# Kernel optimization log

Hardware: AMD Instinct MI355X
Metric: run time of the kernel (lower is better)

The kernel has to match this reference:

```python
import jax, jax.numpy as jnp
import numpy as np

N, E, D, L = 50000, 625000, 128, 7
EPS = 1e-7   # GENConv message epsilon
T = 1.0      # softmax aggregation temperature (learn_t=False)
NUM_ATOM_FEATS, ATOM_VOCAB = 9, 64
NUM_BOND_FEATS, BOND_VOCAB = 3, 8


def setup_inputs() -> dict:
    key = jax.random.key(0)
    ks = jax.random.split(key, 9)
    x = jax.random.randint(ks[0], (N, NUM_ATOM_FEATS), 0, ATOM_VOCAB, dtype=jnp.int32)
    edge_index = jax.random.randint(ks[1], (2, E), 0, N, dtype=jnp.int32)
    edge_attr = jax.random.randint(ks[2], (E, NUM_BOND_FEATS), 0, BOND_VOCAB, dtype=jnp.int32)
    atom_emb = jax.random.normal(ks[3], (NUM_ATOM_FEATS, ATOM_VOCAB, D), dtype=jnp.float32) * 0.1
    bond_emb = jax.random.normal(ks[4], (NUM_BOND_FEATS, BOND_VOCAB, D), dtype=jnp.float32) * 0.1
    W = jax.random.normal(ks[5], (L, D, D), dtype=jnp.float32) / np.sqrt(D).astype(np.float32)
    b = jnp.zeros((L, D), dtype=jnp.float32)
    ln_gamma = jnp.ones((L, D), dtype=jnp.float32)
    ln_beta = jnp.zeros((L, D), dtype=jnp.float32)
    return dict(x=x, edge_index=edge_index, edge_attr=edge_attr,
                atom_emb=atom_emb, bond_emb=bond_emb, W=W, b=b,
                ln_gamma=ln_gamma, ln_beta=ln_beta)


def _layer_norm(h, g, bta):
    mu = jnp.mean(h, axis=-1, keepdims=True)
    var = jnp.var(h, axis=-1, keepdims=True)
    return (h - mu) * jax.lax.rsqrt(var + 1e-5) * g + bta


def _gen_conv(h, src, dst, edge_emb, Wl, bl):
    # GENConv: msg = relu(x_j + e) + eps; softmax aggregation over dst; Linear(x + m)
    msg = jax.nn.relu(h[src] + edge_emb) + EPS                 # [E, D]
    logits = msg * T
    seg_max = jax.ops.segment_max(logits, dst, num_segments=N)  # [N, D]
    seg_max = jnp.where(jnp.isfinite(seg_max), seg_max, 0.0)    # empty segments
    e = jnp.exp(logits - seg_max[dst])                          # [E, D]
    denom = jax.ops.segment_sum(e, dst, num_segments=N)         # [N, D]
    alpha = e / (denom[dst] + 1e-16)
    m = jax.ops.segment_sum(alpha * msg, dst, num_segments=N)   # [N, D]
    return (h + m) @ Wl + bl


def reference(x, edge_index, edge_attr, atom_emb, bond_emb, W, b, ln_gamma, ln_beta):
    src, dst = edge_index[0], edge_index[1]
    # AtomEncoder: sum of per-feature embedding lookups -> [N, D]
    h = jnp.sum(atom_emb[jnp.arange(NUM_ATOM_FEATS)[None, :], x], axis=1)
    # BondEncoder (conv_encode_edge=False: encoded once) -> [E, D]
    edge_emb = jnp.sum(bond_emb[jnp.arange(NUM_BOND_FEATS)[None, :], edge_attr], axis=1)
    # res+ block, dropout=0 (no-op)
    h = _gen_conv(h, src, dst, edge_emb, W[0], b[0])
    for layer in range(1, L):
        h2 = jax.nn.relu(_layer_norm(h, ln_gamma[layer - 1], ln_beta[layer - 1]))
        h = _gen_conv(h2, src, dst, edge_emb, W[layer], b[layer]) + h
    h = _layer_norm(h, ln_gamma[L - 1], ln_beta[L - 1])
    return h
```

## Files before the change

kernel.cpp:

```cpp
#include <hip/hip_runtime.h>
#include <hip/hip_fp16.h>
#include <math.h>


constexpr int D = 128;
constexpr int NA = 9;
constexpr int NB = 3;


__global__ void k_hist(const int* __restrict__ dst, int* __restrict__ deg, int E) {
    int e = blockIdx.x * 256 + threadIdx.x;
    if (e < E) atomicAdd(&deg[dst[e]], 1);
}

__global__ void k_scan_a(const int* __restrict__ deg, int* __restrict__ offs,
                         int* __restrict__ bsum, int N) {
    __shared__ int s[256];
    int i = blockIdx.x * 256 + threadIdx.x;
    int v = (i < N) ? deg[i] : 0;
    s[threadIdx.x] = v;
    __syncthreads();
    for (int d = 1; d < 256; d <<= 1) {
        int add = (threadIdx.x >= d) ? s[threadIdx.x - d] : 0;
        __syncthreads();
        s[threadIdx.x] += add;
        __syncthreads();
    }
    if (i < N) offs[i + 1] = s[threadIdx.x];
    if (threadIdx.x == 255) bsum[blockIdx.x] = s[255];
    if (i == 0) offs[0] = 0;
}

__global__ void k_scan_b(const int* __restrict__ bsum, int* __restrict__ bexc, int nb) {
    __shared__ int s[256];
    int t = threadIdx.x;
    int v = (t < nb) ? bsum[t] : 0;
    s[t] = v;
    __syncthreads();
    for (int d = 1; d < 256; d <<= 1) {
        int add = (t >= d) ? s[t - d] : 0;
        __syncthreads();
        s[t] += add;
        __syncthreads();
    }
    if (t < nb) bexc[t] = s[t] - v;
}

__global__ void k_scan_c(int* __restrict__ offs, const int* __restrict__ bexc, int N) {
    int i = blockIdx.x * 256 + threadIdx.x;
    if (i < N) offs[i + 1] += bexc[blockIdx.x];
}

__global__ void k_fill(const int* __restrict__ src, const int* __restrict__ dst,
                       const int* __restrict__ attr, const int* __restrict__ offs,
                       int* __restrict__ cur, int2* __restrict__ recs, int E) {
    int e = blockIdx.x * 256 + threadIdx.x;
    if (e >= E) return;
    int d = dst[e];
    int pos = offs[d] + atomicAdd(&cur[d], 1);
    int cidx = attr[e * 3] * 64 + attr[e * 3 + 1] * 8 + attr[e * 3 + 2];
    recs[pos] = make_int2(src[e], cidx);
}

__global__ void k_comb(const float* __restrict__ bemb, __half* __restrict__ comb16) {
    int gid = blockIdx.x * 256 + threadIdx.x;
    int c = gid >> 5, q = gid & 31;
    int a0 = c >> 6, a1 = (c >> 3) & 7, a2 = c & 7;
    float4 v0 = *(const float4*)(bemb + (a0)*D + q * 4);
    float4 v1 = *(const float4*)(bemb + (8 + a1) * D + q * 4);
    float4 v2 = *(const float4*)(bemb + (16 + a2) * D + q * 4);
    __half2* c2 = (__half2*)comb16;
    c2[c * 64 + q * 2]     = __floats2half2_rn(v0.x + v1.x + v2.x, v0.y + v1.y + v2.y);
    c2[c * 64 + q * 2 + 1] = __floats2half2_rn(v0.z + v1.z + v2.z, v0.w + v1.w + v2.w);
}


__global__ void k_atom(const int* __restrict__ x, const float* __restrict__ aemb,
                       __half* __restrict__ h16, int N) {
    int wid = (blockIdx.x * blockDim.x + threadIdx.x) >> 6;
    int lane = threadIdx.x & 63;
    if (wid >= N) return;
    const int* xr = x + wid * NA;
    float ax = 0.f, ay = 0.f;
#pragma unroll
    for (int f = 0; f < NA; ++f) {
        int v = xr[f];
        const float2 e = *(const float2*)(aemb + (f * 64 + v) * D + 2 * lane);
        ax += e.x; ay += e.y;
    }
    ((__half2*)h16)[wid * 64 + lane] = __floats2half2_rn(ax, ay);
}


__global__ __launch_bounds__(256) void k_agg(const __half* __restrict__ h16,
                      const int2* __restrict__ recs,
                      const int* __restrict__ offs, const __half* __restrict__ comb16,
                      __half* __restrict__ t16, int N) {
    int wid = (blockIdx.x * blockDim.x + threadIdx.x) >> 6;
    int lane = threadIdx.x & 63;
    if (wid >= N) return;
    int su = __builtin_amdgcn_readfirstlane(offs[wid]);
    int eu = __builtin_amdgcn_readfirstlane(offs[wid + 1]);
    __half2 hm2 = ((const __half2*)h16)[wid * 64 + lane];
    float2 hme = make_float2(__low2float(hm2), __high2float(hm2));
    if (su >= eu) {
        ((__half2*)t16)[wid * 64 + lane] = hm2;
        return;
    }
    constexpr float L2E = 1.4426950408889634f;
    float Sx = 0.f, Sy = 0.f, Wx = 0.f, Wy = 0.f;
    int last = eu - 1;

    const __half2* hrow = (const __half2*)h16 + lane;
    const __half2* crow = (const __half2*)comb16 + lane;

    __half2 ha[4], ca[4], hb[4], cb[4];

    auto loadg = [&](int gb, __half2* hs, __half2* cs) {
#pragma unroll
        for (int i = 0; i < 4; ++i) {
            int idx = gb + i; idx = (idx < last) ? idx : last;
            int2 rr = recs[idx];
            int sj = __builtin_amdgcn_readfirstlane(rr.x);
            int cj = __builtin_amdgcn_readfirstlane(rr.y);
            hs[i] = hrow[sj * 64];
            cs[i] = crow[cj * 64];
        }
    };
    auto compg = [&](int gb, const __half2* hs, const __half2* cs) {
        float px[4], py[4], vx[4], vy[4];
#pragma unroll
        for (int i = 0; i < 4; ++i) {
            float hx = __low2float(hs[i]), hy = __high2float(hs[i]);
            float cx = __low2float(cs[i]), cy = __high2float(cs[i]);
            vx[i] = fmaxf(hx + cx, 0.f) + 1e-7f;
            vy[i] = fmaxf(hy + cy, 0.f) + 1e-7f;
            bool valid = (gb + i) < eu;
            float uxv = valid ? vx[i] * L2E : -INFINITY;
            float uyv = valid ? vy[i] * L2E : -INFINITY;
            px[i] = __builtin_amdgcn_exp2f(uxv);
            py[i] = __builtin_amdgcn_exp2f(uyv);
        }
        Sx += (px[0] + px[1]) + (px[2] + px[3]);
        Sy += (py[0] + py[1]) + (py[2] + py[3]);
        Wx += fmaf(px[0], vx[0], px[1] * vx[1]) + fmaf(px[2], vx[2], px[3] * vx[3]);
        Wy += fmaf(py[0], vy[0], py[1] * vy[1]) + fmaf(py[2], vy[2], py[3] * vy[3]);
    };

    loadg(su, ha, ca);
    loadg(su + 4, hb, cb);
    for (int e = su; e < eu; e += 8) {
        compg(e, ha, ca);
        loadg(e + 8, ha, ca);
        compg(e + 4, hb, cb);
        loadg(e + 12, hb, cb);
    }
    float mx = Wx / (Sx + 1e-16f);
    float my = Wy / (Sy + 1e-16f);
    ((__half2*)t16)[wid * 64 + lane] = __floats2half2_rn(hme.x + mx, hme.y + my);
}


template <int MODE>
__global__ __launch_bounds__(256) void k_gemm(const __half* __restrict__ A16,
                                              const float* __restrict__ Wl,
                                              const float* __restrict__ bl,
                                              const __half* __restrict__ res16,
                                              __half* __restrict__ hres16,
                                              const float* __restrict__ g,
                                              const float* __restrict__ bta,
                                              __half* __restrict__ h16,
                                              float* __restrict__ out,
                                              int N, int useRes) {
    __shared__ float As[32 * 132];
    __shared__ float Bs[32 * 128];
    int tid = threadIdx.x;
    int tx = tid & 15;
    int ty = tid >> 4;
    int m0 = blockIdx.x * 128;

    float acc[8][8];
#pragma unroll
    for (int i = 0; i < 8; ++i)
#pragma unroll
        for (int j = 0; j < 8; ++j) acc[i][j] = 0.f;

    for (int kk0 = 0; kk0 < 128; kk0 += 32) {
#pragma unroll
        for (int it = 0; it < 2; ++it) {
            int lin = it * 256 + tid;
            int node = lin >> 2, kq = lin & 3;
            int gm = m0 + node;
            float4 raw = make_float4(0.f, 0.f, 0.f, 0.f);
            if (gm < N) raw = *(const float4*)(A16 + gm * 128 + kk0 + kq * 8);
            const __half2* hp = (const __half2*)&raw;
#pragma unroll
            for (int j = 0; j < 4; ++j) {
                float2 f = make_float2(__low2float(hp[j]), __high2float(hp[j]));
                As[(kq * 8 + 2 * j) * 132 + node]     = f.x;
                As[(kq * 8 + 2 * j + 1) * 132 + node] = f.y;
            }
        }
#pragma unroll
        for (int it = 0; it < 4; ++it) {
            int lin = it * 256 + tid;
            int k = lin >> 5, jq = lin & 31;
            *(float4*)(Bs + k * 128 + jq * 4) = *(const float4*)(Wl + (kk0 + k) * 128 + jq * 4);
        }
        __syncthreads();
#pragma unroll
        for (int kk = 0; kk < 32; ++kk) {
            float4 a_lo = *(const float4*)(As + kk * 132 + ty * 8);
            float4 a_hi = *(const float4*)(As + kk * 132 + ty * 8 + 4);
            float2 bv[4];
#pragma unroll
            for (int jj = 0; jj < 4; ++jj)
                bv[jj] = *(const float2*)(Bs + kk * 128 + tx * 2 + 32 * jj);
            float am[8] = {a_lo.x, a_lo.y, a_lo.z, a_lo.w,
                           a_hi.x, a_hi.y, a_hi.z, a_hi.w};
#pragma unroll
            for (int i = 0; i < 8; ++i)
#pragma unroll
                for (int jj = 0; jj < 4; ++jj) {
                    acc[i][2 * jj]     = fmaf(am[i], bv[jj].x, acc[i][2 * jj]);
                    acc[i][2 * jj + 1] = fmaf(am[i], bv[jj].y, acc[i][2 * jj + 1]);
                }
        }
        __syncthreads();
    }

    float2 bb[4], gg[4], bt[4];
#pragma unroll
    for (int jj = 0; jj < 4; ++jj) {
        bb[jj] = *(const float2*)(bl + tx * 2 + 32 * jj);
        gg[jj] = *(const float2*)(g + tx * 2 + 32 * jj);
        bt[jj] = *(const float2*)(bta + tx * 2 + 32 * jj);
    }
#pragma unroll
    for (int i = 0; i < 8; ++i) {
        int gm = m0 + ty * 8 + i;
        bool ok = gm < N;
        float o[8];
#pragma unroll
        for (int jj = 0; jj < 4; ++jj) {
            o[2 * jj]     = acc[i][2 * jj] + bb[jj].x;
            o[2 * jj + 1] = acc[i][2 * jj + 1] + bb[jj].y;
        }
        if (useRes && ok) {
#pragma unroll
            for (int jj = 0; jj < 4; ++jj) {
                __half2 rr = *(const __half2*)(res16 + gm * 128 + tx * 2 + 32 * jj);
                o[2 * jj]     += __low2float(rr);
                o[2 * jj + 1] += __high2float(rr);
            }
        }
        if (MODE == 0 && ok) {
#pragma unroll
            for (int jj = 0; jj < 4; ++jj)
                *(__half2*)(hres16 + gm * 128 + tx * 2 + 32 * jj) =
                    __floats2half2_rn(o[2 * jj], o[2 * jj + 1]);
        }
        float s = 0.f, ss = 0.f;
#pragma unroll
        for (int j = 0; j < 8; ++j) { s += o[j]; ss += o[j] * o[j]; }
#pragma unroll
        for (int off = 1; off < 16; off <<= 1) {
            s += __shfl_xor(s, off, 64);
            ss += __shfl_xor(ss, off, 64);
        }
        float mu = s * (1.f / 128.f);
        float var = ss * (1.f / 128.f) - mu * mu;
        float rs = rsqrtf(var + 1e-5f);
        float l[8];
#pragma unroll
        for (int jj = 0; jj < 4; ++jj) {
            l[2 * jj]     = (o[2 * jj] - mu) * rs * gg[jj].x + bt[jj].x;
            l[2 * jj + 1] = (o[2 * jj + 1] - mu) * rs * gg[jj].y + bt[jj].y;
        }
        if (MODE == 0) {
#pragma unroll
            for (int j = 0; j < 8; ++j) l[j] = fmaxf(l[j], 0.f);
            if (ok) {
                __half2* hrow = (__half2*)h16 + gm * 64;
#pragma unroll
                for (int jj = 0; jj < 4; ++jj)
                    hrow[tx + 16 * jj] = __floats2half2_rn(l[2 * jj], l[2 * jj + 1]);
            }
        } else {
            if (ok) {
#pragma unroll
                for (int jj = 0; jj < 4; ++jj)
                    *(float2*)(out + gm * 128 + tx * 2 + 32 * jj) =
                        make_float2(l[2 * jj], l[2 * jj + 1]);
            }
        }
    }
}


extern "C" void kernel_launch(void* const* d_in, const int* in_sizes, int n_in,
                              void* d_out, int out_size, void* d_ws, size_t ws_size,
                              hipStream_t stream) {
    const int*   x    = (const int*)d_in[0];
    const int*   ei   = (const int*)d_in[1];
    const int*   attr = (const int*)d_in[2];
    const float* aemb = (const float*)d_in[3];
    const float* bemb = (const float*)d_in[4];
    const float* Wf   = (const float*)d_in[5];
    const float* bf   = (const float*)d_in[6];
    const float* gam  = (const float*)d_in[7];
    const float* bet  = (const float*)d_in[8];
    float* out = (float*)d_out;

    const int N = in_sizes[0] / NA;
    const int E = in_sizes[1] / 2;
    const int L = in_sizes[5] / (D * D);

    char* ws = (char*)d_ws;
    size_t o = 0;
    auto carve = [&](size_t bytes) -> void* {
        void* p = (void*)(ws + o);
        o += (bytes + 255) & ~(size_t)255;
        return p;
    };
    __half* hres16 = (__half*)carve((size_t)N * D * 2);
    __half* h16    = (__half*)carve((size_t)N * D * 2);
    __half* t16    = (__half*)carve((size_t)N * D * 2);
    int2*   recs   = (int2*)carve((size_t)E * 8);
    __half* comb16 = (__half*)carve(512 * D * 2);
    int*    deg    = (int*)carve((size_t)N * 4);
    int*    cur    = (int*)carve((size_t)N * 4);
    int*    offs   = (int*)carve((size_t)(N + 1) * 4);
    int*    bsum   = (int*)carve(4096);
    int*    bexc   = (int*)carve(4096);

    const int* src = ei;
    const int* dst = ei + E;

    hipMemsetAsync(deg, 0, (size_t)N * 4, stream);
    hipMemsetAsync(cur, 0, (size_t)N * 4, stream);

    int ebl = (E + 255) / 256;
    int nbl = (N + 255) / 256;
    k_comb<<<64, 256, 0, stream>>>(bemb, comb16);
    k_hist<<<ebl, 256, 0, stream>>>(dst, deg, E);
    k_scan_a<<<nbl, 256, 0, stream>>>(deg, offs, bsum, N);
    k_scan_b<<<1, 256, 0, stream>>>(bsum, bexc, nbl);
    k_scan_c<<<nbl, 256, 0, stream>>>(offs, bexc, N);
    k_fill<<<ebl, 256, 0, stream>>>(src, dst, attr, offs, cur, recs, E);

    int wbl = (N * 64 + 255) / 256;
    k_atom<<<wbl, 256, 0, stream>>>(x, aemb, h16, N);

    int gbl = (N + 127) / 128;
    for (int l = 0; l < L; ++l) {
        k_agg<<<wbl, 256, 0, stream>>>(h16, recs, offs, comb16, t16, N);
        if (l == L - 1) {
            k_gemm<1><<<gbl, 256, 0, stream>>>(t16, Wf + l * D * D, bf + l * D,
                                               hres16, hres16,
                                               gam + l * D, bet + l * D, h16, out,
                                               N, 1);
        } else {
            k_gemm<0><<<gbl, 256, 0, stream>>>(t16, Wf + l * D * D, bf + l * D,
                                               hres16, hres16,
                                               gam + l * D, bet + l * D, h16, out,
                                               N, l > 0 ? 1 : 0);
        }
    }
}
```

Before: 673.3 us.

## Replace FP32 SIMT GEMM with FP16 MFMA GEMM using pre-transposed half weights

Rewrites the per-layer linear+LayerNorm kernel to use 16x16x32 FP16 MFMA instructions. Each wave handles 16 nodes and computes all 128 output features from register-resident A fragments, with weights read directly from a pre-transposed FP16 copy instead of staged through shared memory. A new setup kernel converts and transposes all layer weights to half once per launch. This removes the scalar FMA work and the LDS staging, at the cost of FP16 weight precision and uncached global weight reads per wave.

```diff
diff --git a/kernel.cpp b/kernel.cpp
--- a/kernel.cpp
+++ b/kernel.cpp
@@ -6,6 +6,9 @@
 constexpr int D = 128;
 constexpr int NA = 9;
 constexpr int NB = 3;
+
+using half8  = __attribute__((ext_vector_type(8))) _Float16;
+using floatx4 = __attribute__((ext_vector_type(4))) float;
 
 
 __global__ void k_hist(const int* __restrict__ dst, int* __restrict__ deg, int E) {
@@ -72,6 +75,15 @@
     __half2* c2 = (__half2*)comb16;
     c2[c * 64 + q * 2]     = __floats2half2_rn(v0.x + v1.x + v2.x, v0.y + v1.y + v2.y);
     c2[c * 64 + q * 2 + 1] = __floats2half2_rn(v0.z + v1.z + v2.z, v0.w + v1.w + v2.w);
+}
+
+__global__ void k_wt(const float* __restrict__ W, __half* __restrict__ Wt16, int total) {
+    int o = blockIdx.x * 256 + threadIdx.x;
+    if (o >= total) return;
+    int l = o >> 14;
+    int rem = o & 16383;
+    int f = rem >> 7, k = rem & 127;
+    Wt16[o] = __float2half_rn(W[(l << 14) + k * 128 + f]);
 }
 
 
@@ -163,7 +175,7 @@
 
 template <int MODE>
 __global__ __launch_bounds__(256) void k_gemm(const __half* __restrict__ A16,
-                                              const float* __restrict__ Wl,
+                                              const __half* __restrict__ Wt16,
                                               const float* __restrict__ bl,
                                               const __half* __restrict__ res16,
                                               __half* __restrict__ hres16,
@@ -172,127 +184,85 @@
                                               __half* __restrict__ h16,
                                               float* __restrict__ out,
                                               int N, int useRes) {
-    __shared__ float As[32 * 132];
-    __shared__ float Bs[32 * 128];
-    int tid = threadIdx.x;
-    int tx = tid & 15;
-    int ty = tid >> 4;
-    int m0 = blockIdx.x * 128;
-
-    float acc[8][8];
-#pragma unroll
-    for (int i = 0; i < 8; ++i)
-#pragma unroll
-        for (int j = 0; j < 8; ++j) acc[i][j] = 0.f;
-
-    for (int kk0 = 0; kk0 < 128; kk0 += 32) {
-#pragma unroll
-        for (int it = 0; it < 2; ++it) {
-            int lin = it * 256 + tid;
-            int node = lin >> 2, kq = lin & 3;
-            int gm = m0 + node;
-            float4 raw = make_float4(0.f, 0.f, 0.f, 0.f);
-            if (gm < N) raw = *(const float4*)(A16 + gm * 128 + kk0 + kq * 8);
-            const __half2* hp = (const __half2*)&raw;
-#pragma unroll
-            for (int j = 0; j < 4; ++j) {
-                float2 f = make_float2(__low2float(hp[j]), __high2float(hp[j]));
-                As[(kq * 8 + 2 * j) * 132 + node]     = f.x;
-                As[(kq * 8 + 2 * j + 1) * 132 + node] = f.y;
-            }
-        }
-#pragma unroll
-        for (int it = 0; it < 4; ++it) {
-            int lin = it * 256 + tid;
-            int k = lin >> 5, jq = lin & 31;
-            *(float4*)(Bs + k * 128 + jq * 4) = *(const float4*)(Wl + (kk0 + k) * 128 + jq * 4);
-        }
-        __syncthreads();
-#pragma unroll
-        for (int kk = 0; kk < 32; ++kk) {
-            float4 a_lo = *(const float4*)(As + kk * 132 + ty * 8);
-            float4 a_hi = *(const float4*)(As + kk * 132 + ty * 8 + 4);
-            float2 bv[4];
-#pragma unroll
-            for (int jj = 0; jj < 4; ++jj)
-                bv[jj] = *(const float2*)(Bs + kk * 128 + tx * 2 + 32 * jj);
-            float am[8] = {a_lo.x, a_lo.y, a_lo.z, a_lo.w,
-                           a_hi.x, a_hi.y, a_hi.z, a_hi.w};
-#pragma unroll
-            for (int i = 0; i < 8; ++i)
-#pragma unroll
-                for (int jj = 0; jj < 4; ++jj) {
-                    acc[i][2 * jj]     = fmaf(am[i], bv[jj].x, acc[i][2 * jj]);
-                    acc[i][2 * jj + 1] = fmaf(am[i], bv[jj].y, acc[i][2 * jj + 1]);
-                }
-        }
-        __syncthreads();
-    }
-
-    float2 bb[4], gg[4], bt[4];
-#pragma unroll
-    for (int jj = 0; jj < 4; ++jj) {
-        bb[jj] = *(const float2*)(bl + tx * 2 + 32 * jj);
-        gg[jj] = *(const float2*)(g + tx * 2 + 32 * jj);
-        bt[jj] = *(const float2*)(bta + tx * 2 + 32 * jj);
-    }
-#pragma unroll
-    for (int i = 0; i < 8; ++i) {
-        int gm = m0 + ty * 8 + i;
-        bool ok = gm < N;
-        float o[8];
-#pragma unroll
-        for (int jj = 0; jj < 4; ++jj) {
-            o[2 * jj]     = acc[i][2 * jj] + bb[jj].x;
-            o[2 * jj + 1] = acc[i][2 * jj + 1] + bb[jj].y;
-        }
-        if (useRes && ok) {
-#pragma unroll
-            for (int jj = 0; jj < 4; ++jj) {
-                __half2 rr = *(const __half2*)(res16 + gm * 128 + tx * 2 + 32 * jj);
-                o[2 * jj]     += __low2float(rr);
-                o[2 * jj + 1] += __high2float(rr);
-            }
-        }
-        if (MODE == 0 && ok) {
-#pragma unroll
-            for (int jj = 0; jj < 4; ++jj)
-                *(__half2*)(hres16 + gm * 128 + tx * 2 + 32 * jj) =
-                    __floats2half2_rn(o[2 * jj], o[2 * jj + 1]);
-        }
-        float s = 0.f, ss = 0.f;
-#pragma unroll
-        for (int j = 0; j < 8; ++j) { s += o[j]; ss += o[j] * o[j]; }
-#pragma unroll
-        for (int off = 1; off < 16; off <<= 1) {
-            s += __shfl_xor(s, off, 64);
-            ss += __shfl_xor(ss, off, 64);
-        }
-        float mu = s * (1.f / 128.f);
-        float var = ss * (1.f / 128.f) - mu * mu;
-        float rs = rsqrtf(var + 1e-5f);
-        float l[8];
-#pragma unroll
-        for (int jj = 0; jj < 4; ++jj) {
-            l[2 * jj]     = (o[2 * jj] - mu) * rs * gg[jj].x + bt[jj].x;
-            l[2 * jj + 1] = (o[2 * jj + 1] - mu) * rs * gg[jj].y + bt[jj].y;
-        }
+    int lane = threadIdx.x & 63;
+    int wave = threadIdx.x >> 6;
+    int quad = lane >> 4, col = lane & 15;
+    int node = blockIdx.x * 64 + wave * 16 + col;
+    bool nok = node < N;
+    int nc = nok ? node : N - 1;
+
+    const __half* arow = A16 + (size_t)nc * 128;
+    half8 bfrag[4];
+#pragma unroll
+    for (int ks = 0; ks < 4; ++ks)
+        bfrag[ks] = *(const half8*)(arow + ks * 32 + quad * 8);
+
+    floatx4 acc[8];
+#pragma unroll
+    for (int ft = 0; ft < 8; ++ft) acc[ft] = (floatx4){0.f, 0.f, 0.f, 0.f};
+
+#pragma unroll
+    for (int ft = 0; ft < 8; ++ft) {
+        const __half* wrow = Wt16 + (size_t)(ft * 16 + col) * 128;
+#pragma unroll
+        for (int ks = 0; ks < 4; ++ks) {
+            half8 afrag = *(const half8*)(wrow + ks * 32 + quad * 8);
+            acc[ft] = __builtin_amdgcn_mfma_f32_16x16x32_f16(afrag, bfrag[ks],
+                                                             acc[ft], 0, 0, 0);
+        }
+    }
+
+    float s = 0.f, ss = 0.f;
+#pragma unroll
+    for (int ft = 0; ft < 8; ++ft) {
+        int f0 = ft * 16 + quad * 4;
+        float4 bb = *(const float4*)(bl + f0);
+        float o0 = acc[ft][0] + bb.x, o1 = acc[ft][1] + bb.y;
+        float o2 = acc[ft][2] + bb.z, o3 = acc[ft][3] + bb.w;
+        if (useRes) {
+            uint2 rr = *(const uint2*)(res16 + (size_t)nc * 128 + f0);
+            __half2 r01 = *(__half2*)&rr.x, r23 = *(__half2*)&rr.y;
+            o0 += __low2float(r01); o1 += __high2float(r01);
+            o2 += __low2float(r23); o3 += __high2float(r23);
+        }
+        acc[ft][0] = o0; acc[ft][1] = o1; acc[ft][2] = o2; acc[ft][3] = o3;
+        s += (o0 + o1) + (o2 + o3);
+        ss += fmaf(o0, o0, o1 * o1) + fmaf(o2, o2, o3 * o3);
+        if (MODE == 0 && nok) {
+            __half2 h01 = __floats2half2_rn(o0, o1);
+            __half2 h23 = __floats2half2_rn(o2, o3);
+            uint2 pk = make_uint2(*(unsigned*)&h01, *(unsigned*)&h23);
+            *(uint2*)(hres16 + (size_t)node * 128 + f0) = pk;
+        }
+    }
+    s += __shfl_xor(s, 16, 64);  ss += __shfl_xor(ss, 16, 64);
+    s += __shfl_xor(s, 32, 64);  ss += __shfl_xor(ss, 32, 64);
+    float mu = s * (1.f / 128.f);
+    float var = ss * (1.f / 128.f) - mu * mu;
+    float rs = rsqrtf(var + 1e-5f);
+
+#pragma unroll
+    for (int ft = 0; ft < 8; ++ft) {
+        int f0 = ft * 16 + quad * 4;
+        float4 gg = *(const float4*)(g + f0);
+        float4 bt = *(const float4*)(bta + f0);
+        float l0 = (acc[ft][0] - mu) * rs * gg.x + bt.x;
+        float l1 = (acc[ft][1] - mu) * rs * gg.y + bt.y;
+        float l2 = (acc[ft][2] - mu) * rs * gg.z + bt.z;
+        float l3 = (acc[ft][3] - mu) * rs * gg.w + bt.w;
         if (MODE == 0) {
-#pragma unroll
-            for (int j = 0; j < 8; ++j) l[j] = fmaxf(l[j], 0.f);
-            if (ok) {
-                __half2* hrow = (__half2*)h16 + gm * 64;
-#pragma unroll
-                for (int jj = 0; jj < 4; ++jj)
-                    hrow[tx + 16 * jj] = __floats2half2_rn(l[2 * jj], l[2 * jj + 1]);
+            l0 = fmaxf(l0, 0.f); l1 = fmaxf(l1, 0.f);
+            l2 = fmaxf(l2, 0.f); l3 = fmaxf(l3, 0.f);
+            if (nok) {
+                __half2 h01 = __floats2half2_rn(l0, l1);
+                __half2 h23 = __floats2half2_rn(l2, l3);
+                uint2 pk = make_uint2(*(unsigned*)&h01, *(unsigned*)&h23);
+                *(uint2*)(h16 + (size_t)node * 128 + f0) = pk;
             }
         } else {
-            if (ok) {
-#pragma unroll
-                for (int jj = 0; jj < 4; ++jj)
-                    *(float2*)(out + gm * 128 + tx * 2 + 32 * jj) =
-                        make_float2(l[2 * jj], l[2 * jj + 1]);
-            }
+            if (nok)
+                *(float4*)(out + (size_t)node * 128 + f0) =
+                    make_float4(l0, l1, l2, l3);
         }
     }
 }
@@ -328,6 +298,7 @@
     __half* t16    = (__half*)carve((size_t)N * D * 2);
     int2*   recs   = (int2*)carve((size_t)E * 8);
     __half* comb16 = (__half*)carve(512 * D * 2);
+    __half* Wt16   = (__half*)carve((size_t)L * D * D * 2);
     int*    deg    = (int*)carve((size_t)N * 4);
     int*    cur    = (int*)carve((size_t)N * 4);
     int*    offs   = (int*)carve((size_t)(N + 1) * 4);
@@ -343,6 +314,8 @@
     int ebl = (E + 255) / 256;
     int nbl = (N + 255) / 256;
     k_comb<<<64, 256, 0, stream>>>(bemb, comb16);
+    int wtot = L * D * D;
+    k_wt<<<(wtot + 255) / 256, 256, 0, stream>>>(Wf, Wt16, wtot);
     k_hist<<<ebl, 256, 0, stream>>>(dst, deg, E);
     k_scan_a<<<nbl, 256, 0, stream>>>(deg, offs, bsum, N);
     k_scan_b<<<1, 256, 0, stream>>>(bsum, bexc, nbl);
@@ -352,16 +325,16 @@
     int wbl = (N * 64 + 255) / 256;
     k_atom<<<wbl, 256, 0, stream>>>(x, aemb, h16, N);
 
-    int gbl = (N + 127) / 128;
+    int gbl = (N + 63) / 64;
     for (int l = 0; l < L; ++l) {
         k_agg<<<wbl, 256, 0, stream>>>(h16, recs, offs, comb16, t16, N);
         if (l == L - 1) {
-            k_gemm<1><<<gbl, 256, 0, stream>>>(t16, Wf + l * D * D, bf + l * D,
+            k_gemm<1><<<gbl, 256, 0, stream>>>(t16, Wt16 + l * D * D, bf + l * D,
                                                hres16, hres16,
                                                gam + l * D, bet + l * D, h16, out,
                                                N, 1);
         } else {
-            k_gemm<0><<<gbl, 256, 0, stream>>>(t16, Wf + l * D * D, bf + l * D,
+            k_gemm<0><<<gbl, 256, 0, stream>>>(t16, Wt16 + l * D * D, bf + l * D,
                                                hres16, hres16,
                                                gam + l * D, bet + l * D, h16, out,
                                                N, l > 0 ? 1 : 0);
```

Result: no change. 667.4 us (-0.9%).
